# Optimization experiments

Measured on AMD Instinct MI355X. Metric: run time of the kernel, lower is better.

## Reference

```python
import jax, jax.numpy as jnp
import numpy as np

B, S, D, H = 4, 2048, 1024, 16
HD = D // H


def setup_inputs() -> dict:
    key = jax.random.key(0)
    ks = jax.random.split(key, 11)
    s = 1.0 / np.sqrt(D)
    return {
        "query": jax.random.normal(ks[0], (B, S, D), jnp.float32),
        "key": jax.random.normal(ks[1], (B, S, D), jnp.float32),
        "value": jax.random.normal(ks[2], (B, S, D), jnp.float32),
        "Wq": jax.random.normal(ks[3], (D, D), jnp.float32) * s,
        "bq": jax.random.normal(ks[4], (D,), jnp.float32) * s,
        "Wk": jax.random.normal(ks[5], (D, D), jnp.float32) * s,
        "bk": jax.random.normal(ks[6], (D,), jnp.float32) * s,
        "Wv": jax.random.normal(ks[7], (D, D), jnp.float32) * s,
        "bv": jax.random.normal(ks[8], (D,), jnp.float32) * s,
        "Wo": jax.random.normal(ks[9], (D, D), jnp.float32) * s,
        "bo": jax.random.normal(ks[10], (D,), jnp.float32) * s,
    }


def reference(query, key, value, Wq, bq, Wk, bk, Wv, bv, Wo, bo):
    b = query.shape[0]
    # projections (torch Linear: x @ W.T + b)
    q = (query @ Wq.T + bq).reshape(b, -1, H, HD).transpose(0, 2, 1, 3)  # [B,H,S,hd]
    k = (key @ Wk.T + bk).reshape(b, -1, H, HD).transpose(0, 2, 1, 3)
    v = (value @ Wv.T + bv).reshape(b, -1, H, HD).transpose(0, 2, 1, 3)
    scores = jnp.einsum('bhqd,bhkd->bhqk', q, k) / jnp.sqrt(jnp.float32(HD))
    attn = jax.nn.softmax(scores, axis=-1)  # dropout = identity (eval)
    out = jnp.einsum('bhqk,bhkd->bhqd', attn, v)
    out = out.transpose(0, 2, 1, 3).reshape(b, -1, D)
    return out @ Wo.T + bo
```

## Files before the change

### kernel.cpp

```cpp
#include <hip/hip_runtime.h>
#include <stdint.h>

typedef __attribute__((ext_vector_type(8))) short  s16x8;
typedef __attribute__((ext_vector_type(4))) float  f32x4;
typedef __attribute__((ext_vector_type(4))) unsigned short u16x4;

__device__ __forceinline__ unsigned short f2bf(float f) {
  union { float f; uint32_t u; } x; x.f = f;
  uint32_t u = x.u;
  return (unsigned short)((u + 0x7fffu + ((u >> 16) & 1u)) >> 16);
}

__device__ __forceinline__ float fexp2(float x) {
  float r; asm("v_exp_f32 %0, %1" : "=v"(r) : "v"(x)); return r;
}
__device__ __forceinline__ uint32_t cvtpk_bf16(float lo, float hi) {
  uint32_t r; asm("v_cvt_pk_bf16_f32 %0, %1, %2" : "=v"(r) : "v"(lo), "v"(hi)); return r;
}

__device__ __forceinline__ void gload_lds16(const void* g, void* l) {
  __builtin_amdgcn_global_load_lds(
      (const __attribute__((address_space(1))) void*)g,
      (__attribute__((address_space(3))) void*)l, 16, 0, 0);
}

struct CvtJobs {
  const float* src[7];
  unsigned short* dst[7];
  int n4[7];
};
__global__ __launch_bounds__(256) void cvt_all(CvtJobs jobs) {
  const int j = blockIdx.y;
  const float* __restrict__ src = jobs.src[j];
  unsigned short* __restrict__ dst = jobs.dst[j];
  const int n4 = jobs.n4[j];
  const int stride = gridDim.x * blockDim.x;
  for (int i = blockIdx.x * blockDim.x + threadIdx.x; i < n4; i += stride) {
    f32x4 v = *(const f32x4*)(src + (size_t)i * 4);
    u16x4 o = { f2bf(v[0]), f2bf(v[1]), f2bf(v[2]), f2bf(v[3]) };
    *(u16x4*)(dst + (size_t)i * 4) = o;
  }
}

struct GemmJob {
  const unsigned short* A;
  const unsigned short* Bmat;
  const float* bias;
  unsigned short* C;
  int M, N, Nb;
  int bias_row;
  float scale;
};

__device__ __forceinline__ void gemm_core4(const unsigned short* __restrict__ A,
                                           const unsigned short* __restrict__ Bw,
                                           int m0, int n0, int K, char* L,
                                           f32x4 (&acc)[4][4]) {
  const int tid = threadIdx.x;
  const int l = tid & 63;
  const int lr = l & 15, lc = l >> 4;
  const int w = tid >> 6;
  const int wr = w >> 1, wc = w & 1;

  const int srow = tid >> 2;
  const int sc = (tid & 3) ^ ((srow >> 1) & 3);
  const unsigned short* sA1 = A + (size_t)(m0 + srow) * K + sc * 8;
  const unsigned short* sA2 = A + (size_t)(m0 + srow + 64) * K + sc * 8;
  const unsigned short* sB1 = Bw + (size_t)(n0 + srow) * K + sc * 8;
  const unsigned short* sB2 = Bw + (size_t)(n0 + srow + 64) * K + sc * 8;
  char* d1 = L + (size_t)tid * 16;
  char* d2 = d1 + 4096;
  char* d3 = d1 + 8192;
  char* d4 = d1 + 12288;

#define GSTAGE(BUF, KS) { gload_lds16(sA1 + (KS), d1 + (BUF) * 16384); \
                          gload_lds16(sA2 + (KS), d2 + (BUF) * 16384); \
                          gload_lds16(sB1 + (KS), d3 + (BUF) * 16384); \
                          gload_lds16(sB2 + (KS), d4 + (BUF) * 16384); }

  const int s16 = (lc ^ ((lr >> 1) & 3)) * 16;
  int offA[4], offB[4];
#pragma unroll
  for (int i = 0; i < 4; ++i) offA[i] = (wr * 64 + i * 16 + lr) * 64 + s16;
#pragma unroll
  for (int j = 0; j < 4; ++j) offB[j] = 8192 + (wc * 64 + j * 16 + lr) * 64 + s16;

  const int nk = K >> 5;
  GSTAGE(0, 0);
  GSTAGE(1, 32);
  int cur = 0;
  for (int t = 0; t < nk; ++t) {
    if (t < nk - 1) asm volatile("s_waitcnt vmcnt(4)" ::: "memory");
    else            asm volatile("s_waitcnt vmcnt(0)" ::: "memory");
    __builtin_amdgcn_s_barrier();
    if (t < nk - 2) {
      int nb = cur + 2; if (nb >= 3) nb -= 3;
      GSTAGE(nb, (t + 2) * 32);
    }
    const char* Lb = L + cur * 16384;
    s16x8 af[4], bfr[4];
#pragma unroll
    for (int i = 0; i < 4; ++i) af[i] = *(const s16x8*)(Lb + offA[i]);
#pragma unroll
    for (int j = 0; j < 4; ++j) bfr[j] = *(const s16x8*)(Lb + offB[j]);
    __builtin_amdgcn_s_setprio(1);
#pragma unroll
    for (int i = 0; i < 4; ++i)
#pragma unroll
      for (int j = 0; j < 4; ++j)
        acc[i][j] = __builtin_amdgcn_mfma_f32_16x16x32_bf16(af[i], bfr[j], acc[i][j], 0, 0, 0);
    __builtin_amdgcn_s_setprio(0);
    ++cur; if (cur == 3) cur = 0;
  }
#undef GSTAGE
}

__global__ __launch_bounds__(256) void gemm_qkv(GemmJob j0, GemmJob j1, GemmJob j2) {
  __shared__ __align__(16) char L[49152];
  const int f = blockIdx.x;
  const int wid = (f & 7) * 192 + (f >> 3);
  const int job = wid >> 9;
  const int i = wid & 511;
  const GemmJob jb = (job == 0) ? j0 : (job == 1) ? j1 : j2;
  const int m0 = (i / jb.Nb) * 128, n0 = (i % jb.Nb) * 128;
  f32x4 acc[4][4];
#pragma unroll
  for (int i2 = 0; i2 < 4; ++i2)
#pragma unroll
    for (int j2 = 0; j2 < 4; ++j2) acc[i2][j2] = (f32x4){0.f, 0.f, 0.f, 0.f};
  gemm_core4(jb.A, jb.Bmat, m0, n0, 1024, L, acc);
  const int tid = threadIdx.x;
  const int l = tid & 63, w = tid >> 6;
  const int lr = l & 15, lc = l >> 4;
  const int wr = w >> 1, wc = w & 1;
#pragma unroll
  for (int i2 = 0; i2 < 4; ++i2) {
    const int row0 = m0 + wr * 64 + i2 * 16 + lc * 4;
    f32x4 brow;
    if (jb.bias_row) brow = *(const f32x4*)&jb.bias[row0];
#pragma unroll
    for (int j2 = 0; j2 < 4; ++j2) {
      const int col = n0 + wc * 64 + j2 * 16 + lr;
      float bcol = jb.bias_row ? 0.f : jb.bias[col];
#pragma unroll
      for (int r = 0; r < 4; ++r) {
        float v = (acc[i2][j2][r] + (jb.bias_row ? brow[r] : bcol)) * jb.scale;
        jb.C[(size_t)(row0 + r) * jb.N + col] = f2bf(v);
      }
    }
  }
}

__global__ __launch_bounds__(256) void gemm_out(const unsigned short* __restrict__ A,
                                                const unsigned short* __restrict__ Bw,
                                                const float* __restrict__ bias,
                                                float* __restrict__ Cout,
                                                int M, int N, int K) {
  __shared__ __align__(16) char L[49152];
  const int f = blockIdx.x;
  const int wid = (f & 7) * 64 + (f >> 3);
  const int m0 = (wid >> 3) * 128, n0 = (wid & 7) * 128;
  f32x4 acc[4][4];
#pragma unroll
  for (int i = 0; i < 4; ++i)
#pragma unroll
    for (int j = 0; j < 4; ++j) acc[i][j] = (f32x4){0.f, 0.f, 0.f, 0.f};
  gemm_core4(A, Bw, m0, n0, K, L, acc);
  const int tid = threadIdx.x;
  const int l = tid & 63, w = tid >> 6;
  const int lr = l & 15, lc = l >> 4;
  const int wr = w >> 1, wc = w & 1;
#pragma unroll
  for (int i = 0; i < 4; ++i) {
    const int row0 = m0 + wr * 64 + i * 16 + lc * 4;
#pragma unroll
    for (int j = 0; j < 4; ++j) {
      const int col = n0 + wc * 64 + j * 16 + lr;
      float bcol = bias[col];
#pragma unroll
      for (int r = 0; r < 4; ++r)
        Cout[(size_t)(row0 + r) * N + col] = acc[i][j][r] + bcol;
    }
  }
}

__global__ __launch_bounds__(512) void attn_fwd(const unsigned short* __restrict__ qb,
                                                const unsigned short* __restrict__ kb,
                                                const unsigned short* __restrict__ vtb,
                                                unsigned short* __restrict__ ob) {
  __shared__ __align__(16) unsigned short L[3 * 8192];
  const int tid = threadIdx.x;
  const int l = tid & 63, w = tid >> 6;
  const int lr = l & 15, lc = l >> 4;
  const int i0 = blockIdx.x;
  const int wid = (i0 & 7) * 128 + (i0 >> 3);
  const int qx = wid & 15;
  const int h = (wid >> 4) & 15;
  const int b = wid >> 8;
  const int q0 = qx * 128;
  const size_t qkbase = ((size_t)b * 2048) * 1024 + (size_t)h * 64;
  const size_t vtbase = (size_t)(h * 64) * 8192 + (size_t)b * 2048;

  s16x8 aq0, aq1;
  {
    const unsigned short* qp = qb + qkbase + (size_t)(q0 + w * 16 + lr) * 1024 + lc * 8;
    aq0 = *(const s16x8*)qp;
    aq1 = *(const s16x8*)(qp + 32);
  }

  float lsum = 0.f;
  f32x4 oacc[4];
#pragma unroll
  for (int nd = 0; nd < 4; ++nd) oacc[nd] = (f32x4){0.f, 0.f, 0.f, 0.f};

  const int role = w >> 2, wk = w & 3;
  const int rl = l >> 3;
  const int cs = (l & 7) ^ rl;
  const int rA = wk * 16 + rl, rB = rA + 8;
#define RHO(rr) (8 * (((rr) >> 2) & 3) + 4 * (((rr) >> 4) & 1) + ((rr) & 3) + 32 * ((rr) >> 5))
  const unsigned short* sA;
  const unsigned short* sB;
  size_t tstep;
  if (role == 0) {
    sA = kb + qkbase + (size_t)RHO(rA) * 1024 + cs * 8;
    sB = kb + qkbase + (size_t)RHO(rB) * 1024 + cs * 8;
    tstep = (size_t)64 * 1024;
  } else {
    sA = vtb + vtbase + (size_t)rA * 8192 + cs * 8;
    sB = vtb + vtbase + (size_t)rB * 8192 + cs * 8;
    tstep = 64;
  }
#undef RHO
  char* dstL = (char*)L + role * 8192 + wk * 2048 + l * 16;

#define STAGE(BUF, T) {                                              \
    gload_lds16(sA + (size_t)(T) * tstep, dstL + (BUF) * 16384);     \
    gload_lds16(sB + (size_t)(T) * tstep, dstL + (BUF) * 16384 + 1024); }

  int off0[4];
#pragma unroll
  for (int ni = 0; ni < 4; ++ni)
    off0[ni] = (ni * 16 + lr) * 128 + ((lc ^ (lr & 7)) * 16);

  STAGE(0, 0);
  STAGE(1, 1);

  int cur = 0;
  for (int t = 0; t < 32; ++t) {
    if (t < 31) asm volatile("s_waitcnt vmcnt(2)" ::: "memory");
    else        asm volatile("s_waitcnt vmcnt(0)" ::: "memory");
    __builtin_amdgcn_s_barrier();
    if (t < 30) {
      int nb = cur + 2; if (nb >= 3) nb -= 3;
      STAGE(nb, t + 2);
    }
    const char* Lb = (const char*)L + cur * 16384;

    f32x4 sf[4];
    __builtin_amdgcn_s_setprio(1);
#pragma unroll
    for (int ni = 0; ni < 4; ++ni) {
      s16x8 k0 = *(const s16x8*)(Lb + off0[ni]);
      s16x8 k1 = *(const s16x8*)(Lb + (off0[ni] ^ 64));
      f32x4 z = (f32x4){0.f, 0.f, 0.f, 0.f};
      z = __builtin_amdgcn_mfma_f32_16x16x32_bf16(k0, aq0, z, 0, 0, 0);
      z = __builtin_amdgcn_mfma_f32_16x16x32_bf16(k1, aq1, z, 0, 0, 0);
      sf[ni] = z;
    }
    __builtin_amdgcn_s_setprio(0);

    union { uint32_t u[4]; s16x8 v; } pa0u, pa1u;
#pragma unroll
    for (int ni = 0; ni < 4; ++ni) {
      float p0 = fexp2(sf[ni][0]);
      float p1 = fexp2(sf[ni][1]);
      float p2 = fexp2(sf[ni][2]);
      float p3 = fexp2(sf[ni][3]);
      lsum += (p0 + p1) + (p2 + p3);
      uint32_t w0 = cvtpk_bf16(p0, p1);
      uint32_t w1 = cvtpk_bf16(p2, p3);
      if (ni < 2) { pa0u.u[ni * 2] = w0; pa0u.u[ni * 2 + 1] = w1; }
      else        { pa1u.u[(ni - 2) * 2] = w0; pa1u.u[(ni - 2) * 2 + 1] = w1; }
    }

    __builtin_amdgcn_s_setprio(1);
#pragma unroll
    for (int nd = 0; nd < 4; ++nd) {
      s16x8 v0 = *(const s16x8*)(Lb + 8192 + off0[nd]);
      s16x8 v1 = *(const s16x8*)(Lb + 8192 + (off0[nd] ^ 64));
      oacc[nd] = __builtin_amdgcn_mfma_f32_16x16x32_bf16(pa0u.v, v0, oacc[nd], 0, 0, 0);
      oacc[nd] = __builtin_amdgcn_mfma_f32_16x16x32_bf16(pa1u.v, v1, oacc[nd], 0, 0, 0);
    }
    __builtin_amdgcn_s_setprio(0);

    ++cur; if (cur == 3) cur = 0;
  }

  lsum += __shfl_xor(lsum, 16, 64);
  lsum += __shfl_xor(lsum, 32, 64);
  float linv[4];
#pragma unroll
  for (int r = 0; r < 4; ++r) linv[r] = 1.f / __shfl(lsum, lc * 4 + r, 64);
#pragma unroll
  for (int nd = 0; nd < 4; ++nd)
#pragma unroll
    for (int r = 0; r < 4; ++r) {
      int qrow = q0 + w * 16 + lc * 4 + r;
      ob[qkbase + (size_t)qrow * 1024 + nd * 16 + lr] = f2bf(oacc[nd][r] * linv[r]);
    }
#undef STAGE
}

extern "C" void kernel_launch(void* const* d_in, const int* in_sizes, int n_in,
                              void* d_out, int out_size, void* d_ws, size_t ws_size,
                              hipStream_t stream) {
  const float* query = (const float*)d_in[0];
  const float* key_  = (const float*)d_in[1];
  const float* value = (const float*)d_in[2];
  const float* Wq = (const float*)d_in[3];
  const float* bq = (const float*)d_in[4];
  const float* Wk = (const float*)d_in[5];
  const float* bk = (const float*)d_in[6];
  const float* Wv = (const float*)d_in[7];
  const float* bv = (const float*)d_in[8];
  const float* Wo = (const float*)d_in[9];
  const float* bo = (const float*)d_in[10];

  const int MS = 4 * 2048;
  const int D = 1024;
  const size_t NX = (size_t)MS * D;
  const size_t NW = (size_t)D * D;

  const size_t need = (6 * NX + 4 * NW) * 2;
  if (ws_size < need) return;

  unsigned short* ws  = (unsigned short*)d_ws;
  unsigned short* xq  = ws;
  unsigned short* xk  = xq + NX;
  unsigned short* xv  = xk + NX;
  unsigned short* qb_ = xv + NX;
  unsigned short* kb_ = qb_ + NX;
  unsigned short* vtb = kb_ + NX;
  unsigned short* wqb = vtb + NX;
  unsigned short* wkb = wqb + NW;
  unsigned short* wvb = wkb + NW;
  unsigned short* wob = wvb + NW;
  unsigned short* attn = xq;

  CvtJobs cj;
  cj.src[0] = query; cj.dst[0] = xq;  cj.n4[0] = (int)(NX / 4);
  cj.src[1] = key_;  cj.dst[1] = xk;  cj.n4[1] = (int)(NX / 4);
  cj.src[2] = value; cj.dst[2] = xv;  cj.n4[2] = (int)(NX / 4);
  cj.src[3] = Wq;    cj.dst[3] = wqb; cj.n4[3] = (int)(NW / 4);
  cj.src[4] = Wk;    cj.dst[4] = wkb; cj.n4[4] = (int)(NW / 4);
  cj.src[5] = Wv;    cj.dst[5] = wvb; cj.n4[5] = (int)(NW / 4);
  cj.src[6] = Wo;    cj.dst[6] = wob; cj.n4[6] = (int)(NW / 4);
  cvt_all<<<dim3(1024, 7), 256, 0, stream>>>(cj);

  const float qscale = 0.18033688f;
  GemmJob jq = { xq,  wqb, bq, qb_, MS, D,  D / 128,  0, qscale };
  GemmJob jk = { xk,  wkb, bk, kb_, MS, D,  D / 128,  0, 1.f };
  GemmJob jv = { wvb, xv,  bv, vtb, D,  MS, MS / 128, 1, 1.f };
  gemm_qkv<<<dim3(1536), 256, 0, stream>>>(jq, jk, jv);

  attn_fwd<<<dim3(1024), 512, 0, stream>>>(qb_, kb_, vtb, attn);

  gemm_out<<<dim3(512), 256, 0, stream>>>(attn, wob, bo, (float*)d_out, MS, D, D);
}
```

Measured before the change: 206.4 us.

## Fuse fp32-to-bf16 activation conversion into QKV projection GEMM loads

```diff
diff --git a/kernel.cpp b/kernel.cpp
--- a/kernel.cpp
+++ b/kernel.cpp
@@ -4,6 +4,7 @@
 typedef __attribute__((ext_vector_type(8))) short  s16x8;
 typedef __attribute__((ext_vector_type(4))) float  f32x4;
 typedef __attribute__((ext_vector_type(4))) unsigned short u16x4;
+typedef __attribute__((ext_vector_type(4))) uint32_t u32x4;
 
 __device__ __forceinline__ unsigned short f2bf(float f) {
   union { float f; uint32_t u; } x; x.f = f;
@@ -25,9 +26,9 @@
 }
 
 struct CvtJobs {
-  const float* src[7];
-  unsigned short* dst[7];
-  int n4[7];
+  const float* src[4];
+  unsigned short* dst[4];
+  int n4[4];
 };
 __global__ __launch_bounds__(256) void cvt_all(CvtJobs jobs) {
   const int j = blockIdx.y;
@@ -42,16 +43,6 @@
   }
 }
 
-struct GemmJob {
-  const unsigned short* A;
-  const unsigned short* Bmat;
-  const float* bias;
-  unsigned short* C;
-  int M, N, Nb;
-  int bias_row;
-  float scale;
-};
-
 __device__ __forceinline__ void gemm_core4(const unsigned short* __restrict__ A,
                                            const unsigned short* __restrict__ Bw,
                                            int m0, int n0, int K, char* L,
@@ -115,20 +106,118 @@
 #undef GSTAGE
 }
 
-__global__ __launch_bounds__(256) void gemm_qkv(GemmJob j0, GemmJob j1, GemmJob j2) {
+template <int SIDE>
+__device__ __forceinline__ void gemm_core4f(const float* __restrict__ F,
+                                            const unsigned short* __restrict__ H,
+                                            int f0, int h0, int K, char* L,
+                                            f32x4 (&acc)[4][4]) {
+  const int tid = threadIdx.x;
+  const int l = tid & 63;
+  const int lr = l & 15, lc = l >> 4;
+  const int w = tid >> 6;
+  const int wr = w >> 1, wc = w & 1;
+  const int srow = tid >> 2;
+  const int sc = (tid & 3) ^ ((srow >> 1) & 3);
+
+  const int fbase = (SIDE == 1) ? 0 : 8192;
+  const int hbase = (SIDE == 1) ? 8192 : 0;
+
+  const float* f1 = F + (size_t)(f0 + srow) * K + (tid & 3) * 8;
+  const float* f2 = f1 + (size_t)64 * K;
+  const unsigned short* h1 = H + (size_t)(h0 + srow) * K + sc * 8;
+  const unsigned short* h2 = h1 + (size_t)64 * K;
+  char* hd1 = L + hbase + tid * 16;
+  char* hd2 = hd1 + 4096;
+  char* wd1 = L + fbase + srow * 64 + (((tid & 3) ^ ((srow >> 1) & 3)) << 4);
+  char* wd2 = wd1 + 4096;
+
+  f32x4 ra0, ra1, ra2, ra3;
+#define RL(KS) { ra0 = *(const f32x4*)(f1 + (KS)); ra1 = *(const f32x4*)(f1 + (KS) + 4); \
+                 ra2 = *(const f32x4*)(f2 + (KS)); ra3 = *(const f32x4*)(f2 + (KS) + 4); }
+#define GLH(BUF, KS) { gload_lds16(h1 + (KS), hd1 + (BUF) * 16384); \
+                       gload_lds16(h2 + (KS), hd2 + (BUF) * 16384); }
+#define WRF(BUF) { u32x4 t1 = { cvtpk_bf16(ra0[0], ra0[1]), cvtpk_bf16(ra0[2], ra0[3]),   \
+                                cvtpk_bf16(ra1[0], ra1[1]), cvtpk_bf16(ra1[2], ra1[3]) }; \
+                   *(u32x4*)(wd1 + (BUF) * 16384) = t1;                                   \
+                   u32x4 t2 = { cvtpk_bf16(ra2[0], ra2[1]), cvtpk_bf16(ra2[2], ra2[3]),   \
+                                cvtpk_bf16(ra3[0], ra3[1]), cvtpk_bf16(ra3[2], ra3[3]) }; \
+                   *(u32x4*)(wd2 + (BUF) * 16384) = t2; }
+
+  const int s16 = (lc ^ ((lr >> 1) & 3)) * 16;
+  int offA[4], offB[4];
+#pragma unroll
+  for (int i = 0; i < 4; ++i) offA[i] = (wr * 64 + i * 16 + lr) * 64 + s16;
+#pragma unroll
+  for (int j = 0; j < 4; ++j) offB[j] = 8192 + (wc * 64 + j * 16 + lr) * 64 + s16;
+
+  const int nk = K >> 5;
+  RL(0); GLH(0, 0);
+  asm volatile("s_waitcnt vmcnt(2)" ::: "memory");
+  WRF(0);
+  asm volatile("s_waitcnt lgkmcnt(0)" ::: "memory");
+  RL(32); GLH(1, 32);
+
+  int cur = 0;
+  for (int t = 0; t < nk; ++t) {
+    if (t < nk - 1) asm volatile("s_waitcnt vmcnt(2)" ::: "memory");
+    else            asm volatile("s_waitcnt vmcnt(0)" ::: "memory");
+    __builtin_amdgcn_s_barrier();
+    if (t + 1 < nk) {
+      int nb = cur + 1; if (nb >= 3) nb -= 3;
+      WRF(nb);
+    }
+    if (t + 2 < nk) {
+      int nb2 = cur + 2; if (nb2 >= 3) nb2 -= 3;
+      RL((t + 2) * 32);
+      GLH(nb2, (t + 2) * 32);
+    }
+    const char* Lb = L + cur * 16384;
+    s16x8 af[4], bfr[4];
+#pragma unroll
+    for (int i = 0; i < 4; ++i) af[i] = *(const s16x8*)(Lb + offA[i]);
+#pragma unroll
+    for (int j = 0; j < 4; ++j) bfr[j] = *(const s16x8*)(Lb + offB[j]);
+    asm volatile("s_waitcnt lgkmcnt(0)" ::: "memory");
+    __builtin_amdgcn_s_setprio(1);
+#pragma unroll
+    for (int i = 0; i < 4; ++i)
+#pragma unroll
+      for (int j = 0; j < 4; ++j)
+        acc[i][j] = __builtin_amdgcn_mfma_f32_16x16x32_bf16(af[i], bfr[j], acc[i][j], 0, 0, 0);
+    __builtin_amdgcn_s_setprio(0);
+    ++cur; if (cur == 3) cur = 0;
+  }
+#undef RL
+#undef GLH
+#undef WRF
+}
+
+struct GemmJobF {
+  const float* F;
+  const unsigned short* Hm;
+  const float* bias;
+  unsigned short* C;
+  int N, Nb;
+  int side;
+  int bias_row;
+  float scale;
+};
+
+__global__ __launch_bounds__(256) void gemm_qkv(GemmJobF j0, GemmJobF j1, GemmJobF j2) {
   __shared__ __align__(16) char L[49152];
   const int f = blockIdx.x;
   const int wid = (f & 7) * 192 + (f >> 3);
   const int job = wid >> 9;
   const int i = wid & 511;
-  const GemmJob jb = (job == 0) ? j0 : (job == 1) ? j1 : j2;
+  const GemmJobF jb = (job == 0) ? j0 : (job == 1) ? j1 : j2;
   const int m0 = (i / jb.Nb) * 128, n0 = (i % jb.Nb) * 128;
   f32x4 acc[4][4];
 #pragma unroll
   for (int i2 = 0; i2 < 4; ++i2)
 #pragma unroll
     for (int j2 = 0; j2 < 4; ++j2) acc[i2][j2] = (f32x4){0.f, 0.f, 0.f, 0.f};
-  gemm_core4(jb.A, jb.Bmat, m0, n0, 1024, L, acc);
+  if (jb.side == 1) gemm_core4f<1>(jb.F, jb.Hm, m0, n0, 1024, L, acc);
+  else              gemm_core4f<2>(jb.F, jb.Hm, n0, m0, 1024, L, acc);
   const int tid = threadIdx.x;
   const int l = tid & 63, w = tid >> 6;
   const int lr = l & 15, lc = l >> 4;
@@ -331,36 +420,30 @@
   const size_t NX = (size_t)MS * D;
   const size_t NW = (size_t)D * D;
 
-  const size_t need = (6 * NX + 4 * NW) * 2;
+  const size_t need = (4 * NX + 4 * NW) * 2;
   if (ws_size < need) return;
 
   unsigned short* ws  = (unsigned short*)d_ws;
-  unsigned short* xq  = ws;
-  unsigned short* xk  = xq + NX;
-  unsigned short* xv  = xk + NX;
-  unsigned short* qb_ = xv + NX;
+  unsigned short* qb_ = ws;
   unsigned short* kb_ = qb_ + NX;
   unsigned short* vtb = kb_ + NX;
-  unsigned short* wqb = vtb + NX;
+  unsigned short* attn = vtb + NX;
+  unsigned short* wqb = attn + NX;
   unsigned short* wkb = wqb + NW;
   unsigned short* wvb = wkb + NW;
   unsigned short* wob = wvb + NW;
-  unsigned short* attn = xq;
 
   CvtJobs cj;
-  cj.src[0] = query; cj.dst[0] = xq;  cj.n4[0] = (int)(NX / 4);
-  cj.src[1] = key_;  cj.dst[1] = xk;  cj.n4[1] = (int)(NX / 4);
-  cj.src[2] = value; cj.dst[2] = xv;  cj.n4[2] = (int)(NX / 4);
-  cj.src[3] = Wq;    cj.dst[3] = wqb; cj.n4[3] = (int)(NW / 4);
-  cj.src[4] = Wk;    cj.dst[4] = wkb; cj.n4[4] = (int)(NW / 4);
-  cj.src[5] = Wv;    cj.dst[5] = wvb; cj.n4[5] = (int)(NW / 4);
-  cj.src[6] = Wo;    cj.dst[6] = wob; cj.n4[6] = (int)(NW / 4);
-  cvt_all<<<dim3(1024, 7), 256, 0, stream>>>(cj);
+  cj.src[0] = Wq; cj.dst[0] = wqb; cj.n4[0] = (int)(NW / 4);
+  cj.src[1] = Wk; cj.dst[1] = wkb; cj.n4[1] = (int)(NW / 4);
+  cj.src[2] = Wv; cj.dst[2] = wvb; cj.n4[2] = (int)(NW / 4);
+  cj.src[3] = Wo; cj.dst[3] = wob; cj.n4[3] = (int)(NW / 4);
+  cvt_all<<<dim3(256, 4), 256, 0, stream>>>(cj);
 
   const float qscale = 0.18033688f;
-  GemmJob jq = { xq,  wqb, bq, qb_, MS, D,  D / 128,  0, qscale };
-  GemmJob jk = { xk,  wkb, bk, kb_, MS, D,  D / 128,  0, 1.f };
-  GemmJob jv = { wvb, xv,  bv, vtb, D,  MS, MS / 128, 1, 1.f };
+  GemmJobF jq = { query, wqb, bq, qb_, D,  D / 128,  1, 0, qscale };
+  GemmJobF jk = { key_,  wkb, bk, kb_, D,  D / 128,  1, 0, 1.f };
+  GemmJobF jv = { value, wvb, bv, vtb, MS, MS / 128, 2, 1, 1.f };
   gemm_qkv<<<dim3(1536), 256, 0, stream>>>(jq, jk, jv);
 
   attn_fwd<<<dim3(1024), 512, 0, stream>>>(qb_, kb_, vtb, attn);
```

After: 206.7 us. No clear change (+0.1%).
